# Kernel optimization log

Measured on AMD Instinct MI355X. Metric: run time of the kernel, lower is better.

Reference implementation:

```python
import jax, jax.numpy as jnp
import numpy as np
from jax import lax

H = 192; W = 192; C = 256; N = H * W; E = 294912; K = 289; DSIG = 1
SLOPE = 0.01
EPS = 1e-5


def leaky(x):
    return jnp.where(x >= 0, x, SLOPE * x)


def conv2d(x, w, pad, groups):
    return lax.conv_general_dilated(
        x, w, (1, 1), [(pad, pad), (pad, pad)],
        dimension_numbers=('NCHW', 'OIHW', 'NCHW'),
        feature_group_count=groups)


def bn2d(x, g, b):
    # BatchNorm2d with track_running_stats=False -> always batch stats (biased var)
    m = x.mean(axis=(0, 2, 3), keepdims=True)
    v = x.var(axis=(0, 2, 3), keepdims=True)
    return (x - m) / jnp.sqrt(v + EPS) * g.reshape(1, -1, 1, 1) + b.reshape(1, -1, 1, 1)


def conv_batch(x, w, g, b, pad, groups):
    # nn.Sequential(LeakyReLU(0.01), Conv2d(bias=False), BatchNorm2d)
    return bn2d(conv2d(leaky(x), w, pad, groups), g, b)


def bn1d(x, g, b):
    m = x.mean(axis=0)
    v = x.var(axis=0)
    return (x - m) / jnp.sqrt(v + EPS) * g + b


def setup_inputs() -> dict:
    key = jax.random.key(0)
    ks = jax.random.split(key, 20)
    X = jax.random.normal(ks[0], (N, C), dtype=jnp.float32)
    src = jax.random.randint(ks[1], (E,), 0, N)
    dst = jax.random.randint(ks[2], (E,), 0, N)
    k1 = jax.random.randint(ks[3], (E,), 0, K)
    k2 = jax.random.randint(ks[4], (E,), 0, K)
    InfoIdx = jnp.stack([src, k1, dst, k2], axis=1).astype(jnp.int64)
    edgmsk = (jax.random.uniform(ks[5], (E, 1)) < 0.9).astype(jnp.float32)
    s = 0.05
    inp = {
        'X': X, 'InfoIdx': InfoIdx, 'edgmsk': edgmsk,
        # PPM: depthwise 17x17 conv_batch then 1x1 conv_batch
        'ppm_w0': jax.random.normal(ks[6], (C, 1, 17, 17), jnp.float32) * s,
        'ppm_g0': jnp.ones((C,), jnp.float32), 'ppm_b0': jnp.zeros((C,), jnp.float32),
        'ppm_w1': jax.random.normal(ks[7], (C, C, 1, 1), jnp.float32) * s,
        'ppm_g1': jnp.ones((C,), jnp.float32), 'ppm_b1': jnp.zeros((C,), jnp.float32),
        # FFN_1: two 1x1 conv_batch
        'ffn1_w0': jax.random.normal(ks[8], (C, C, 1, 1), jnp.float32) * s,
        'ffn1_g0': jnp.ones((C,), jnp.float32), 'ffn1_b0': jnp.zeros((C,), jnp.float32),
        'ffn1_w1': jax.random.normal(ks[9], (C, C, 1, 1), jnp.float32) * s,
        'ffn1_g1': jnp.ones((C,), jnp.float32), 'ffn1_b1': jnp.zeros((C,), jnp.float32),
        # Dis: Linear(C,C) -> LeakyReLU -> Linear(C, 289)
        'dis_w1': jax.random.normal(ks[10], (C, C), jnp.float32) * s,
        'dis_b1': jnp.zeros((C,), jnp.float32),
        'dis_w2': jax.random.normal(ks[11], (K * DSIG, C), jnp.float32) * s,
        'dis_b2': jnp.zeros((K * DSIG,), jnp.float32),
        # BatchNorm1d
        'bn_g': jnp.ones((C,), jnp.float32), 'bn_b': jnp.zeros((C,), jnp.float32),
        # FFN_2 = DoubleConv: depthwise-expand 3x3 (groups=C, out=4C) then 1x1
        'ffn2_w0': jax.random.normal(ks[12], (4 * C, 1, 3, 3), jnp.float32) * s,
        'ffn2_g0': jnp.ones((4 * C,), jnp.float32), 'ffn2_b0': jnp.zeros((4 * C,), jnp.float32),
        'ffn2_w1': jax.random.normal(ks[13], (C, 4 * C, 1, 1), jnp.float32) * s,
        'ffn2_g1': jnp.ones((C,), jnp.float32), 'ffn2_b1': jnp.zeros((C,), jnp.float32),
    }
    return inp


def reference(X, InfoIdx, edgmsk,
              ppm_w0, ppm_g0, ppm_b0, ppm_w1, ppm_g1, ppm_b1,
              ffn1_w0, ffn1_g0, ffn1_b0, ffn1_w1, ffn1_g1, ffn1_b1,
              dis_w1, dis_b1, dis_w2, dis_b2, bn_g, bn_b,
              ffn2_w0, ffn2_g0, ffn2_b0, ffn2_w1, ffn2_g1, ffn2_b1):
    src_idx = InfoIdx[:, 0]
    dst_idx = InfoIdx[:, 2]
    # [N,C] -> [1,C,H,W]
    img = X.T.reshape(1, C, H, W)
    # PPM residual
    t = conv_batch(img, ppm_w0, ppm_g0, ppm_b0, pad=8, groups=C)
    t = conv_batch(t, ppm_w1, ppm_g1, ppm_b1, pad=0, groups=1)
    img = img + t
    # FFN_1 residual
    t = conv_batch(img, ffn1_w0, ffn1_g0, ffn1_b0, pad=0, groups=1)
    t = conv_batch(t, ffn1_w1, ffn1_g1, ffn1_b1, pad=0, groups=1)
    img = img + t
    Xn = img.reshape(C, N).T  # [N, C]
    # Dis MLP -> signal [N, 289, d_signal]
    h = leaky(Xn @ dis_w1.T + dis_b1)
    signal = (h @ dis_w2.T + dis_b2).reshape(N, K, DSIG)
    # edge gather + exp/clamp score
    s_src = signal[src_idx, InfoIdx[:, 1]]  # [E, 1]
    s_dst = signal[dst_idx, InfoIdx[:, 3]]  # [E, 1]
    aij = jnp.exp(jnp.clip(s_src + s_dst, -5.0, 5.0)) * edgmsk  # [E, 1]
    # two scatter-sum reductions to dst nodes
    A_sum = jax.ops.segment_sum(aij, dst_idx, num_segments=N)  # [N, 1]
    XA_sum = jax.ops.segment_sum(Xn[src_idx] * aij, dst_idx, num_segments=N)  # [N, C]
    X_trans = XA_sum / (A_sum + 1e-5)
    Xn = Xn + bn1d(X_trans, bn_g, bn_b)
    # FFN_2 = DoubleConv with residual skip
    img = Xn.T.reshape(1, C, H, W)
    t = conv_batch(img, ffn2_w0, ffn2_g0, ffn2_b0, pad=1, groups=C)
    t = conv_batch(t, ffn2_w1, ffn2_g1, ffn2_b1, pad=0, groups=1)
    out = t + img
    return out.reshape(C, N).T  # final bg.ndata['X'], [N, C]
```

## Files before the change

kernel.cpp:

```cpp
#include <hip/hip_runtime.h>
#include <cstddef>

#define HW 192
#define NP 36864
#define CH 256
#define EDGES 294912
#define KSIG 289
#define SLOPE 0.01f
#define BNEPS 1e-5f
#define PADW 208
#define PADSZ (PADW * PADW)

typedef unsigned short u16;
typedef __attribute__((ext_vector_type(8))) short bf16x8;
typedef __attribute__((ext_vector_type(4))) float f32x4;

__device__ __forceinline__ float leaky(float x) { return x >= 0.f ? x : SLOPE * x; }
__device__ __forceinline__ u16 f2bf(float x) {
  unsigned u = __float_as_uint(x);
  unsigned r = (u + 0x7fffu + ((u >> 16) & 1u)) >> 16;
  return (u16)r;
}
__device__ __forceinline__ float bf2f(unsigned h) { return __uint_as_float(h << 16); }
__device__ __forceinline__ void bnss(const float* sums, const float* sqs,
                                     const float* g, const float* b, int k,
                                     float& s, float& h) {
  float mean = sums[k] * (1.f / NP);
  float var = sqs[k] * (1.f / NP) - mean * mean;
  s = g[k] * rsqrtf(var + BNEPS);
  h = b[k] - mean * s;
}

__global__ __launch_bounds__(256) void k_transpose_pad(const float* __restrict__ src,
                                                       float* __restrict__ dst,
                                                       u16* __restrict__ pad) {
  __shared__ float tile[32][33];
  int s0 = blockIdx.x * 32, r0 = blockIdx.y * 32;
  int tx = threadIdx.x & 31, ty = threadIdx.x >> 5;
#pragma unroll
  for (int j = 0; j < 4; j++)
    tile[ty + 8 * j][tx] = src[(size_t)(r0 + ty + 8 * j) * CH + s0 + tx];
  __syncthreads();
  int n = r0 + tx;
  int y = n / HW, x = n - y * HW;
#pragma unroll
  for (int j = 0; j < 4; j++) {
    int c = s0 + ty + 8 * j;
    float v = tile[tx][ty + 8 * j];
    dst[(size_t)c * NP + n] = v;
    pad[(size_t)c * PADSZ + (y + 8) * PADW + x + 8] = f2bf(leaky(v));
  }
}

__global__ __launch_bounds__(256) void k_mkT(const float* __restrict__ w,
                                             u16* __restrict__ Tg) {
  int c = blockIdx.x;
  const float* wc = w + c * 289;
  u16* tc = Tg + (size_t)c * 8704;
  for (int i = threadIdx.x; i < 8704; i += 256) {
    int ky = i >> 9, rem = i & 511, n = rem >> 5, k = rem & 31;
    int kx = k - n;
    float v = (kx >= 0 && kx < 17) ? wc[ky * 17 + kx] : 0.f;
    tc[i] = f2bf(v);
  }
}

__global__ __launch_bounds__(256) void k_cvtW(const float* __restrict__ pw1,
                                              const float* __restrict__ f1w0,
                                              const float* __restrict__ f1w1,
                                              const float* __restrict__ dw1,
                                              const float* __restrict__ dw2,
                                              const float* __restrict__ f2w1,
                                              u16* __restrict__ out) {
  int i = blockIdx.x * 256 + threadIdx.x;
  float v;
  if (i < 65536) v = pw1[i];
  else if (i < 131072) v = f1w0[i - 65536];
  else if (i < 196608) v = f1w1[i - 131072];
  else if (i < 262144) v = dw1[i - 196608];
  else if (i < 360448) { int j = i - 262144; v = (j < KSIG * 256) ? dw2[j] : 0.f; }
  else v = f2w1[i - 360448];
  out[i] = f2bf(v);
}

__global__ __launch_bounds__(256) void k_stats_bf(const u16* __restrict__ Xr,
                                                  float* __restrict__ sums,
                                                  float* __restrict__ sqs) {
  int row = blockIdx.x;
  int t = threadIdx.x;
  const uint4* p = (const uint4*)(Xr + (size_t)row * NP);
  float s = 0.f, q = 0.f;
  for (int i = t; i < NP / 8; i += 256) {
    uint4 v = p[i];
    unsigned w[4] = {v.x, v.y, v.z, v.w};
#pragma unroll
    for (int j = 0; j < 4; j++) {
      float a = bf2f(w[j] & 0xffffu), c = bf2f(w[j] >> 16);
      s += a + c; q += a * a + c * c;
    }
  }
  __shared__ float ss[256], qq[256];
  ss[t] = s; qq[t] = q;
  __syncthreads();
  for (int d = 128; d > 0; d >>= 1) {
    if (t < d) { ss[t] += ss[t + d]; qq[t] += qq[t + d]; }
    __syncthreads();
  }
  if (t == 0) { sums[row] = ss[0]; sqs[row] = qq[0]; }
}

__global__ __launch_bounds__(256) void k_cvtT(const float* __restrict__ in,
                                              u16* __restrict__ outT, int M) {
  __shared__ float tile[32][65];
  int n0 = blockIdx.x * 64, k0 = blockIdx.y * 32;
  int t = threadIdx.x;
#pragma unroll
  for (int i = 0; i < 2; i++) {
    int ci = i * 256 + t;
    int k = ci >> 4, cg = (ci & 15) * 4;
    float4 v = *(const float4*)&in[(size_t)(k0 + k) * NP + n0 + cg];
    tile[k][cg] = v.x; tile[k][cg + 1] = v.y; tile[k][cg + 2] = v.z; tile[k][cg + 3] = v.w;
  }
  __syncthreads();
  int n = t >> 2, kg = (t & 3) * 8;
  uint4 o;
  o.x = (unsigned)f2bf(tile[kg + 0][n]) | ((unsigned)f2bf(tile[kg + 1][n]) << 16);
  o.y = (unsigned)f2bf(tile[kg + 2][n]) | ((unsigned)f2bf(tile[kg + 3][n]) << 16);
  o.z = (unsigned)f2bf(tile[kg + 4][n]) | ((unsigned)f2bf(tile[kg + 5][n]) << 16);
  o.w = (unsigned)f2bf(tile[kg + 6][n]) | ((unsigned)f2bf(tile[kg + 7][n]) << 16);
  *(uint4*)&outT[(size_t)(n0 + n) * M + k0 + kg] = o;
}

__global__ __launch_bounds__(256) void k_cvtT_bf(const u16* __restrict__ in,
                                                 u16* __restrict__ outT,
                                                 const float* __restrict__ sums,
                                                 const float* __restrict__ sqs,
                                                 const float* __restrict__ g,
                                                 const float* __restrict__ b, int M) {
  __shared__ float tile[32][65];
  int n0 = blockIdx.x * 64, k0 = blockIdx.y * 32;
  int t = threadIdx.x;
  int k = t >> 3, cg = (t & 7) * 8;
  float s, h; bnss(sums, sqs, g, b, k0 + k, s, h);
  uint4 v = *(const uint4*)&in[(size_t)(k0 + k) * NP + n0 + cg];
  unsigned w[4] = {v.x, v.y, v.z, v.w};
#pragma unroll
  for (int j = 0; j < 4; j++) {
    tile[k][cg + 2 * j]     = leaky(fmaf(bf2f(w[j] & 0xffffu), s, h));
    tile[k][cg + 2 * j + 1] = leaky(fmaf(bf2f(w[j] >> 16), s, h));
  }
  __syncthreads();
  int n = t >> 2, kg = (t & 3) * 8;
  uint4 o;
  o.x = (unsigned)f2bf(tile[kg + 0][n]) | ((unsigned)f2bf(tile[kg + 1][n]) << 16);
  o.y = (unsigned)f2bf(tile[kg + 2][n]) | ((unsigned)f2bf(tile[kg + 3][n]) << 16);
  o.z = (unsigned)f2bf(tile[kg + 4][n]) | ((unsigned)f2bf(tile[kg + 5][n]) << 16);
  o.w = (unsigned)f2bf(tile[kg + 6][n]) | ((unsigned)f2bf(tile[kg + 7][n]) << 16);
  *(uint4*)&outT[(size_t)(n0 + n) * M + k0 + kg] = o;
}

__global__ __launch_bounds__(256) void k_fuse1(const float* __restrict__ base,
                                               const u16* __restrict__ raw,
                                               const float* __restrict__ sums,
                                               const float* __restrict__ sqs,
                                               const float* __restrict__ g,
                                               const float* __restrict__ b,
                                               float* __restrict__ img2,
                                               u16* __restrict__ outT) {
  __shared__ float tile[32][65];
  int n0 = blockIdx.x * 64, k0 = blockIdx.y * 32;
  int t = threadIdx.x;
#pragma unroll
  for (int i = 0; i < 2; i++) {
    int ci = i * 256 + t;
    int k = ci >> 4, cg = (ci & 15) * 4;
    float s, h; bnss(sums, sqs, g, b, k0 + k, s, h);
    size_t idx = (size_t)(k0 + k) * NP + n0 + cg;
    float4 bv = *(const float4*)&base[idx];
    uint2 rv = *(const uint2*)&raw[idx];
    float r0 = bf2f(rv.x & 0xffffu), r1 = bf2f(rv.x >> 16);
    float r2 = bf2f(rv.y & 0xffffu), r3 = bf2f(rv.y >> 16);
    float4 o;
    o.x = bv.x + fmaf(r0, s, h); o.y = bv.y + fmaf(r1, s, h);
    o.z = bv.z + fmaf(r2, s, h); o.w = bv.w + fmaf(r3, s, h);
    *(float4*)&img2[idx] = o;
    tile[k][cg]     = leaky(o.x);
    tile[k][cg + 1] = leaky(o.y);
    tile[k][cg + 2] = leaky(o.z);
    tile[k][cg + 3] = leaky(o.w);
  }
  __syncthreads();
  int n = t >> 2, kg = (t & 3) * 8;
  uint4 o;
  o.x = (unsigned)f2bf(tile[kg + 0][n]) | ((unsigned)f2bf(tile[kg + 1][n]) << 16);
  o.y = (unsigned)f2bf(tile[kg + 2][n]) | ((unsigned)f2bf(tile[kg + 3][n]) << 16);
  o.z = (unsigned)f2bf(tile[kg + 4][n]) | ((unsigned)f2bf(tile[kg + 5][n]) << 16);
  o.w = (unsigned)f2bf(tile[kg + 6][n]) | ((unsigned)f2bf(tile[kg + 7][n]) << 16);
  *(uint4*)&outT[(size_t)(n0 + n) * CH + k0 + kg] = o;
}

__global__ __launch_bounds__(256) void k_fuse2(const float* __restrict__ base,
                                               const u16* __restrict__ raw,
                                               const float* __restrict__ sums,
                                               const float* __restrict__ sqs,
                                               const float* __restrict__ g,
                                               const float* __restrict__ b,
                                               float* __restrict__ XnT,
                                               u16* __restrict__ outT) {
  __shared__ float tile[32][65];
  int n0 = blockIdx.x * 64, k0 = blockIdx.y * 32;
  int t = threadIdx.x;
#pragma unroll
  for (int i = 0; i < 2; i++) {
    int ci = i * 256 + t;
    int k = ci >> 4, cg = (ci & 15) * 4;
    float s, h; bnss(sums, sqs, g, b, k0 + k, s, h);
    size_t idx = (size_t)(k0 + k) * NP + n0 + cg;
    float4 bv = *(const float4*)&base[idx];
    uint2 rv = *(const uint2*)&raw[idx];
    float r0 = bf2f(rv.x & 0xffffu), r1 = bf2f(rv.x >> 16);
    float r2 = bf2f(rv.y & 0xffffu), r3 = bf2f(rv.y >> 16);
    tile[k][cg]     = bv.x + fmaf(r0, s, h);
    tile[k][cg + 1] = bv.y + fmaf(r1, s, h);
    tile[k][cg + 2] = bv.z + fmaf(r2, s, h);
    tile[k][cg + 3] = bv.w + fmaf(r3, s, h);
  }
  __syncthreads();
  int n = t >> 2, kg = (t & 3) * 8;
  float4 f0 = {tile[kg + 0][n], tile[kg + 1][n], tile[kg + 2][n], tile[kg + 3][n]};
  float4 f1 = {tile[kg + 4][n], tile[kg + 5][n], tile[kg + 6][n], tile[kg + 7][n]};
  *(float4*)&XnT[(size_t)(n0 + n) * CH + k0 + kg] = f0;
  *(float4*)&XnT[(size_t)(n0 + n) * CH + k0 + kg + 4] = f1;
  uint4 o;
  o.x = (unsigned)f2bf(f0.x) | ((unsigned)f2bf(f0.y) << 16);
  o.y = (unsigned)f2bf(f0.z) | ((unsigned)f2bf(f0.w) << 16);
  o.z = (unsigned)f2bf(f1.x) | ((unsigned)f2bf(f1.y) << 16);
  o.w = (unsigned)f2bf(f1.z) | ((unsigned)f2bf(f1.w) << 16);
  *(uint4*)&outT[(size_t)(n0 + n) * CH + k0 + kg] = o;
}

__global__ __launch_bounds__(256) void k_mgemm(const u16* __restrict__ A,
                                               const u16* __restrict__ Bt,
                                               float* __restrict__ Outf,
                                               u16* __restrict__ Outb,
                                               const float* __restrict__ bias,
                                               int K, int Mstore, int actout) {
  __shared__ u16 As[128 * 32];
  __shared__ u16 Bs[128 * 32];
  int t = threadIdx.x;
  int lane = t & 63, wave = t >> 6;
  int wm = (wave >> 1) * 64, wn = (wave & 1) * 64;
  int m0 = blockIdx.y * 128, n0 = blockIdx.x * 128;
  int r = lane & 15, q = lane >> 4;
  f32x4 acc[4][4];
#pragma unroll
  for (int a = 0; a < 4; a++)
#pragma unroll
    for (int b = 0; b < 4; b++) acc[a][b] = (f32x4){0.f, 0.f, 0.f, 0.f};

  for (int k0 = 0; k0 < K; k0 += 32) {
#pragma unroll
    for (int i = 0; i < 2; i++) {
      int cc = t + i * 256;
      int mm = cc >> 2, kq = (cc & 3) * 8;
      uint4 av = *(const uint4*)&A[(size_t)(m0 + mm) * K + k0 + kq];
      uint4 bv = *(const uint4*)&Bt[(size_t)(n0 + mm) * K + k0 + kq];
      *(uint4*)&As[mm * 32 + kq] = av;
      *(uint4*)&Bs[mm * 32 + kq] = bv;
    }
    __syncthreads();
    bf16x8 af[4], bfr[4];
#pragma unroll
    for (int mt = 0; mt < 4; mt++)
      af[mt] = *(const bf16x8*)&As[(wm + mt * 16 + r) * 32 + q * 8];
#pragma unroll
    for (int nt = 0; nt < 4; nt++)
      bfr[nt] = *(const bf16x8*)&Bs[(wn + nt * 16 + r) * 32 + q * 8];
#pragma unroll
    for (int mt = 0; mt < 4; mt++)
#pragma unroll
      for (int nt = 0; nt < 4; nt++)
        acc[mt][nt] = __builtin_amdgcn_mfma_f32_16x16x32_bf16(af[mt], bfr[nt], acc[mt][nt], 0, 0, 0);
    __syncthreads();
  }
#pragma unroll
  for (int mt = 0; mt < 4; mt++) {
    int mrow = m0 + wm + mt * 16 + q * 4;
#pragma unroll
    for (int i = 0; i < 4; i++) {
      int m = mrow + i;
      if (m >= Mstore) continue;
      float bs = bias ? bias[m] : 0.f;
#pragma unroll
      for (int nt = 0; nt < 4; nt++) {
        float v = acc[mt][nt][i] + bs;
        if (actout) v = leaky(v);
        size_t oi = (size_t)m * NP + n0 + wn + nt * 16 + r;
        if (Outb) Outb[oi] = f2bf(v); else Outf[oi] = v;
      }
    }
  }
}

__global__ __launch_bounds__(256) void k_dwconv17(const u16* __restrict__ pad,
                                                  const u16* __restrict__ Tg,
                                                  u16* __restrict__ outb) {
  int c = blockIdx.y;
  int tile = blockIdx.x;
  int ty0 = (tile / 3) * 64, tx0 = (tile % 3) * 64;
  __shared__ u16 smIn[80 * 88];
  __shared__ u16 smT[17 * 16 * 40];
  const u16* pc = pad + (size_t)c * PADSZ;
  for (int cc = threadIdx.x; cc < 800; cc += 256) {
    int rr = cc / 10, j = cc - rr * 10;
    uint4 v = *(const uint4*)(pc + (ty0 + rr) * PADW + tx0 + j * 8);
    *(uint4*)(smIn + rr * 88 + j * 8) = v;
  }
  const u16* tc = Tg + (size_t)c * 8704;
  for (int cc = threadIdx.x; cc < 1088; cc += 256) {
    int rr = cc >> 2, j = cc & 3;
    uint4 v = *(const uint4*)(tc + rr * 32 + j * 8);
    *(uint4*)(smT + rr * 40 + j * 8) = v;
  }
  __syncthreads();
  int lane = threadIdx.x & 63, wave = threadIdx.x >> 6;
  int wy = wave * 16;
  int r = lane & 15, q = lane >> 4;
  f32x4 acc[4];
#pragma unroll
  for (int xt = 0; xt < 4; xt++) acc[xt] = (f32x4){0.f, 0.f, 0.f, 0.f};
#pragma unroll
  for (int ky = 0; ky < 17; ky++) {
    bf16x8 bfrag = *(const bf16x8*)&smT[(ky * 16 + r) * 40 + q * 8];
    int rowA = wy + r + ky;
#pragma unroll
    for (int xt = 0; xt < 4; xt++) {
      bf16x8 afrag = *(const bf16x8*)&smIn[rowA * 88 + xt * 16 + q * 8];
      acc[xt] = __builtin_amdgcn_mfma_f32_16x16x32_bf16(afrag, bfrag, acc[xt], 0, 0, 0);
    }
  }
  u16* oc = outb + (size_t)c * NP;
#pragma unroll
  for (int xt = 0; xt < 4; xt++) {
    int x = tx0 + xt * 16 + r;
#pragma unroll
    for (int i = 0; i < 4; i++) {
      int y = ty0 + wy + q * 4 + i;
      oc[y * HW + x] = f2bf(acc[xt][i]);
    }
  }
}

__global__ __launch_bounds__(256) void k_conv3x4(const float* __restrict__ in,
                                                 const float* __restrict__ w,
                                                 u16* __restrict__ out) {
  int wave = threadIdx.x >> 6, lane = threadIdx.x & 63;
  int c = blockIdx.y;
  int y = blockIdx.x * 4 + wave;
  const float* wc = w + (size_t)(4 * c) * 9;
  float wr[36];
#pragma unroll
  for (int k = 0; k < 36; k++) wr[k] = wc[k];
  float acc[4][3];
#pragma unroll
  for (int oc = 0; oc < 4; oc++)
#pragma unroll
    for (int s = 0; s < 3; s++) acc[oc][s] = 0.f;
  const float* base = in + (size_t)c * NP;
#pragma unroll
  for (int ky = 0; ky < 3; ky++) {
    int ry = y + ky - 1;
    if (ry < 0 || ry >= HW) continue;
    const float* rp = base + ry * HW;
    float a0 = leaky(rp[lane]);
    float a1 = leaky(rp[64 + lane]);
    float a2 = leaky(rp[128 + lane]);
    float e0 = __shfl(a0, 63), e1 = __shfl(a1, 63);
    float b1 = __shfl(a1, 0),  b2 = __shfl(a2, 0);
    float l0 = __shfl_up(a0, 1); if (lane == 0) l0 = 0.f;
    float l1 = __shfl_up(a1, 1); if (lane == 0) l1 = e0;
    float l2 = __shfl_up(a2, 1); if (lane == 0) l2 = e1;
    float r0 = __shfl_down(a0, 1); if (lane == 63) r0 = b1;
    float r1 = __shfl_down(a1, 1); if (lane == 63) r1 = b2;
    float r2 = __shfl_down(a2, 1); if (lane == 63) r2 = 0.f;
#pragma unroll
    for (int oc = 0; oc < 4; oc++) {
      float w0 = wr[oc * 9 + ky * 3], w1 = wr[oc * 9 + ky * 3 + 1], w2 = wr[oc * 9 + ky * 3 + 2];
      acc[oc][0] = fmaf(w0, l0, fmaf(w1, a0, fmaf(w2, r0, acc[oc][0])));
      acc[oc][1] = fmaf(w0, l1, fmaf(w1, a1, fmaf(w2, r1, acc[oc][1])));
      acc[oc][2] = fmaf(w0, l2, fmaf(w1, a2, fmaf(w2, r2, acc[oc][2])));
    }
  }
  size_t ob = (size_t)(4 * c) * NP + (size_t)y * HW + lane;
#pragma unroll
  for (int oc = 0; oc < 4; oc++) {
    out[ob + (size_t)oc * NP]       = f2bf(acc[oc][0]);
    out[ob + (size_t)oc * NP + 64]  = f2bf(acc[oc][1]);
    out[ob + (size_t)oc * NP + 128] = f2bf(acc[oc][2]);
  }
}

__global__ __launch_bounds__(256) void k_edge(const int* __restrict__ info,
                                              const float* __restrict__ msk,
                                              const float* __restrict__ sig,
                                              float* __restrict__ aij,
                                              int* __restrict__ counts) {
  int e = blockIdx.x * 256 + threadIdx.x;
  int4 ii = ((const int4*)info)[e];
  float s = sig[(size_t)ii.y * NP + ii.x] + sig[(size_t)ii.w * NP + ii.z];
  s = fminf(fmaxf(s, -5.f), 5.f);
  aij[e] = expf(s) * msk[e];
  atomicAdd(&counts[ii.z], 1);
}

__global__ __launch_bounds__(256) void k_scan1(const int* __restrict__ counts,
                                               int* __restrict__ offsets,
                                               int* __restrict__ bsum) {
  __shared__ int sm[256];
  int t = threadIdx.x;
  int i = blockIdx.x * 256 + t;
  int v = counts[i];
  sm[t] = v;
  __syncthreads();
  for (int d = 1; d < 256; d <<= 1) {
    int add = (t >= d) ? sm[t - d] : 0;
    __syncthreads();
    sm[t] += add;
    __syncthreads();
  }
  offsets[i] = sm[t] - v;
  if (t == 255) bsum[blockIdx.x] = sm[255];
}
__global__ __launch_bounds__(256) void k_scan2(const int* __restrict__ bsum,
                                               int* __restrict__ boff) {
  __shared__ int sm[256];
  int t = threadIdx.x;
  int v = (t < 144) ? bsum[t] : 0;
  sm[t] = v;
  __syncthreads();
  for (int d = 1; d < 256; d <<= 1) {
    int add = (t >= d) ? sm[t - d] : 0;
    __syncthreads();
    sm[t] += add;
    __syncthreads();
  }
  boff[t] = sm[t] - v;
}
__global__ __launch_bounds__(256) void k_scan3(int* __restrict__ offsets,
                                               const int* __restrict__ boff,
                                               int* __restrict__ cursor) {
  int i = blockIdx.x * 256 + threadIdx.x;
  int o = offsets[i] + boff[blockIdx.x];
  offsets[i] = o;
  cursor[i] = o;
  if (i == 0) offsets[NP] = EDGES;
}
__global__ __launch_bounds__(256) void k_scatter(const int* __restrict__ info,
                                                 int* __restrict__ cursor,
                                                 int* __restrict__ sorted) {
  int e = blockIdx.x * 256 + threadIdx.x;
  int d = info[4 * e + 2];
  int pos = atomicAdd(&cursor[d], 1);
  sorted[pos] = e;
}

__global__ __launch_bounds__(256) void k_agg(const int* __restrict__ offsets,
                                             const int* __restrict__ sorted,
                                             const float* __restrict__ aij,
                                             const int* __restrict__ info,
                                             const u16* __restrict__ XnBf,
                                             float* __restrict__ Xtr) {
  int wave = threadIdx.x >> 6, lane = threadIdx.x & 63;
  int node = blockIdx.x * 4 + wave;
  int o0 = offsets[node], o1 = offsets[node + 1];
  float ax = 0.f, ay = 0.f, az = 0.f, aw = 0.f, asum = 0.f;
  for (int i = o0; i < o1; i++) {
    int e = sorted[i];
    float a = aij[e];
    int s = info[4 * e];
    uint2 v = ((const uint2*)(XnBf + (size_t)s * CH))[lane];
    ax = fmaf(a, bf2f(v.x & 0xffffu), ax);
    ay = fmaf(a, bf2f(v.x >> 16), ay);
    az = fmaf(a, bf2f(v.y & 0xffffu), az);
    aw = fmaf(a, bf2f(v.y >> 16), aw);
    asum += a;
  }
  float inv = 1.f / (asum + 1e-5f);
  float4 o = {ax * inv, ay * inv, az * inv, aw * inv};
  ((float4*)(Xtr + (size_t)node * CH))[lane] = o;
}

__global__ __launch_bounds__(256) void k_colstats(const float* __restrict__ Xt,
                                                  float* __restrict__ sums,
                                                  float* __restrict__ sqs) {
  int c = threadIdx.x;
  float s = 0.f, q = 0.f;
  for (int n = blockIdx.x; n < NP; n += gridDim.x) {
    float v = Xt[(size_t)n * CH + c];
    s += v; q += v * v;
  }
  atomicAdd(&sums[c], s);
  atomicAdd(&sqs[c], q);
}

__global__ __launch_bounds__(256) void k_mkimg4(const float* __restrict__ Xn,
                                                const float* __restrict__ Xtr,
                                                const float* __restrict__ sums,
                                                const float* __restrict__ sqs,
                                                const float* __restrict__ g,
                                                const float* __restrict__ b,
                                                float* __restrict__ img4) {
  __shared__ float tile[32][33];
  int c0 = blockIdx.x * 32, n0 = blockIdx.y * 32;
  int tx = threadIdx.x & 31, ty = threadIdx.x >> 5;
  int c = c0 + tx;
  float s, h; bnss(sums, sqs, g, b, c, s, h);
#pragma unroll
  for (int j = 0; j < 4; j++) {
    size_t idx = (size_t)(n0 + ty + 8 * j) * CH + c;
    tile[ty + 8 * j][tx] = Xn[idx] + fmaf(Xtr[idx], s, h);
  }
  __syncthreads();
#pragma unroll
  for (int j = 0; j < 4; j++) {
    int cc = c0 + ty + 8 * j;
    img4[(size_t)cc * NP + n0 + tx] = tile[tx][ty + 8 * j];
  }
}

__global__ __launch_bounds__(256) void k_final(const u16* __restrict__ raw5,
                                               const float* __restrict__ img4,
                                               const float* __restrict__ sums,
                                               const float* __restrict__ sqs,
                                               const float* __restrict__ g,
                                               const float* __restrict__ b,
                                               float* __restrict__ out) {
  __shared__ float tile[32][33];
  int n0 = blockIdx.x * 32, c0 = blockIdx.y * 32;
  int tx = threadIdx.x & 31, ty = threadIdx.x >> 5;
#pragma unroll
  for (int j = 0; j < 4; j++) {
    int c = c0 + ty + 8 * j;
    float s, h; bnss(sums, sqs, g, b, c, s, h);
    size_t idx = (size_t)c * NP + n0 + tx;
    tile[ty + 8 * j][tx] = fmaf(bf2f(raw5[idx]), s, h) + img4[idx];
  }
  __syncthreads();
#pragma unroll
  for (int j = 0; j < 4; j++) {
    int n = n0 + ty + 8 * j;
    out[(size_t)n * CH + c0 + tx] = tile[tx][ty + 8 * j];
  }
}

extern "C" void kernel_launch(void* const* d_in, const int* in_sizes, int n_in,
                              void* d_out, int out_size, void* d_ws, size_t ws_size,
                              hipStream_t stream) {
  (void)in_sizes; (void)n_in; (void)out_size; (void)ws_size;
  const float* X    = (const float*)d_in[0];
  const int*   info = (const int*)d_in[1];
  const float* msk  = (const float*)d_in[2];
  const float* pw0  = (const float*)d_in[3];
  const float* pg0  = (const float*)d_in[4];
  const float* pb0  = (const float*)d_in[5];
  const float* pw1  = (const float*)d_in[6];
  const float* pg1  = (const float*)d_in[7];
  const float* pb1  = (const float*)d_in[8];
  const float* f1w0 = (const float*)d_in[9];
  const float* f1g0 = (const float*)d_in[10];
  const float* f1b0 = (const float*)d_in[11];
  const float* f1w1 = (const float*)d_in[12];
  const float* f1g1 = (const float*)d_in[13];
  const float* f1b1 = (const float*)d_in[14];
  const float* dw1  = (const float*)d_in[15];
  const float* db1  = (const float*)d_in[16];
  const float* dw2  = (const float*)d_in[17];
  const float* db2  = (const float*)d_in[18];
  const float* bng  = (const float*)d_in[19];
  const float* bnb  = (const float*)d_in[20];
  const float* f2w0 = (const float*)d_in[21];
  const float* f2g0 = (const float*)d_in[22];
  const float* f2b0 = (const float*)d_in[23];
  const float* f2w1 = (const float*)d_in[24];
  const float* f2g1 = (const float*)d_in[25];
  const float* f2b1 = (const float*)d_in[26];
  float* out = (float*)d_out;

  float* ws = (float*)d_ws;
  float* sum0 = ws + 0;    float* sq0 = ws + 256;
  float* sum1 = ws + 512;  float* sq1 = ws + 768;
  float* sum2 = ws + 1024; float* sq2 = ws + 1280;
  float* sum3 = ws + 1536; float* sq3 = ws + 1792;
  float* sum5 = ws + 2048; float* sq5 = ws + 2304;
  float* sumT = ws + 2560; float* sqT = ws + 2816;
  float* sum4 = ws + 3072; float* sq4 = ws + 4096;
  int* counts  = (int*)(ws + 8192);
  int* offsets = (int*)(ws + 45056);
  int* cursor  = (int*)(ws + 82176);
  int* bsum    = (int*)(ws + 119296);
  int* boff    = (int*)(ws + 119552);
  int* sorted  = (int*)(ws + 131072);
  float* aij   = ws + 425984;
  const size_t S = (size_t)NP * CH;
  float* slotD = ws + 720896;
  float* slotB = slotD + S;
  float* slotA = slotB + S;
  float* slotC = slotA + S;
  u16* bfB  = (u16*)(slotC + S);
  u16* bfH  = bfB + S;
  float* sigT = (float*)(bfH + S);
  u16* bfW  = (u16*)(sigT + (size_t)KSIG * NP);
  u16* Ppad = (u16*)slotC;
  u16* Tg   = (u16*)slotD;
  u16* raw4bf  = (u16*)slotB;
  u16* bfT1024 = bfB;
  u16* raw5bf  = (u16*)slotD;

  hipMemsetAsync(ws, 0, 5120 * sizeof(float), stream);
  hipMemsetAsync(counts, 0, NP * sizeof(int), stream);
  hipMemsetAsync(Ppad, 0, (size_t)PADSZ * CH * sizeof(u16), stream);

  dim3 b256(256);
  k_cvtW<<<2432, b256, 0, stream>>>(pw1, f1w0, f1w1, dw1, dw2, f2w1, bfW);
  k_mkT<<<CH, b256, 0, stream>>>(pw0, Tg);
  k_transpose_pad<<<dim3(CH / 32, NP / 32), b256, 0, stream>>>(X, slotA, Ppad);
  k_dwconv17<<<dim3(9, CH), b256, 0, stream>>>(Ppad, Tg, bfH);
  k_stats_bf<<<CH, b256, 0, stream>>>(bfH, sum0, sq0);
  k_cvtT_bf<<<dim3(NP / 64, 8), b256, 0, stream>>>(bfH, bfB, sum0, sq0, pg0, pb0, CH);
  k_mgemm<<<dim3(NP / 128, 2), b256, 0, stream>>>(bfW, bfB, nullptr, bfH, nullptr, CH, CH, 0);
  k_stats_bf<<<CH, b256, 0, stream>>>(bfH, sum1, sq1);
  k_fuse1<<<dim3(NP / 64, 8), b256, 0, stream>>>(slotA, bfH, sum1, sq1, pg1, pb1, slotD, bfB);
  k_mgemm<<<dim3(NP / 128, 2), b256, 0, stream>>>(bfW + 65536, bfB, nullptr, bfH, nullptr, CH, CH, 0);
  k_stats_bf<<<CH, b256, 0, stream>>>(bfH, sum2, sq2);
  k_cvtT_bf<<<dim3(NP / 64, 8), b256, 0, stream>>>(bfH, bfB, sum2, sq2, f1g0, f1b0, CH);
  k_mgemm<<<dim3(NP / 128, 2), b256, 0, stream>>>(bfW + 131072, bfB, nullptr, bfH, nullptr, CH, CH, 0);
  k_stats_bf<<<CH, b256, 0, stream>>>(bfH, sum3, sq3);
  k_fuse2<<<dim3(NP / 64, 8), b256, 0, stream>>>(slotD, bfH, sum3, sq3, f1g1, f1b1, slotA, bfB);
  k_mgemm<<<dim3(NP / 128, 2), b256, 0, stream>>>(bfW + 196608, bfB, slotC, nullptr, db1, CH, CH, 1);
  k_cvtT<<<dim3(NP / 64, 8), b256, 0, stream>>>(slotC, bfH, CH);
  k_mgemm<<<dim3(NP / 128, 3), b256, 0, stream>>>(bfW + 262144, bfH, sigT, nullptr, db2, CH, KSIG, 0);
  k_edge<<<EDGES / 256, b256, 0, stream>>>(info, msk, sigT, aij, counts);
  k_scan1<<<NP / 256, b256, 0, stream>>>(counts, offsets, bsum);
  k_scan2<<<1, b256, 0, stream>>>(bsum, boff);
  k_scan3<<<NP / 256, b256, 0, stream>>>(offsets, boff, cursor);
  k_scatter<<<EDGES / 256, b256, 0, stream>>>(info, cursor, sorted);
  k_agg<<<NP / 4, b256, 0, stream>>>(offsets, sorted, aij, info, bfB, slotD);
  k_colstats<<<288, b256, 0, stream>>>(slotD, sumT, sqT);
  k_mkimg4<<<dim3(CH / 32, NP / 32), b256, 0, stream>>>(slotA, slotD, sumT, sqT, bng, bnb, slotC);
  k_conv3x4<<<dim3(48, CH), b256, 0, stream>>>(slotC, f2w0, raw4bf);
  k_stats_bf<<<1024, b256, 0, stream>>>(raw4bf, sum4, sq4);
  k_cvtT_bf<<<dim3(NP / 64, 32), b256, 0, stream>>>(raw4bf, bfT1024, sum4, sq4, f2g0, f2b0, 1024);
  k_mgemm<<<dim3(NP / 128, 2), b256, 0, stream>>>(bfW + 360448, bfT1024, nullptr, raw5bf, nullptr, 1024, CH, 0);
  k_stats_bf<<<CH, b256, 0, stream>>>(raw5bf, sum5, sq5);
  k_final<<<dim3(NP / 32, CH / 32), b256, 0, stream>>>(raw5bf, slotC, sum5, sq5, f2g1, f2b1, out);
}
```

Baseline: 676.6 us.

## Presort edge src/weights in scatter, widen aggregation loads, store X_trans as bf16

```diff
diff --git a/kernel.cpp b/kernel.cpp
--- a/kernel.cpp
+++ b/kernel.cpp
@@ -456,47 +456,78 @@
   if (i == 0) offsets[NP] = EDGES;
 }
 __global__ __launch_bounds__(256) void k_scatter(const int* __restrict__ info,
+                                                 const float* __restrict__ aij,
                                                  int* __restrict__ cursor,
-                                                 int* __restrict__ sorted) {
+                                                 int* __restrict__ srcs,
+                                                 float* __restrict__ aijw) {
   int e = blockIdx.x * 256 + threadIdx.x;
-  int d = info[4 * e + 2];
-  int pos = atomicAdd(&cursor[d], 1);
-  sorted[pos] = e;
+  int4 ii = ((const int4*)info)[e];
+  int pos = atomicAdd(&cursor[ii.z], 1);
+  srcs[pos] = ii.x;
+  aijw[pos] = aij[e];
 }
 
 __global__ __launch_bounds__(256) void k_agg(const int* __restrict__ offsets,
-                                             const int* __restrict__ sorted,
-                                             const float* __restrict__ aij,
-                                             const int* __restrict__ info,
+                                             const int* __restrict__ srcs,
+                                             const float* __restrict__ aijw,
                                              const u16* __restrict__ XnBf,
-                                             float* __restrict__ Xtr) {
+                                             u16* __restrict__ XtrBf) {
   int wave = threadIdx.x >> 6, lane = threadIdx.x & 63;
   int node = blockIdx.x * 4 + wave;
   int o0 = offsets[node], o1 = offsets[node + 1];
-  float ax = 0.f, ay = 0.f, az = 0.f, aw = 0.f, asum = 0.f;
-  for (int i = o0; i < o1; i++) {
-    int e = sorted[i];
-    float a = aij[e];
-    int s = info[4 * e];
-    uint2 v = ((const uint2*)(XnBf + (size_t)s * CH))[lane];
-    ax = fmaf(a, bf2f(v.x & 0xffffu), ax);
-    ay = fmaf(a, bf2f(v.x >> 16), ay);
-    az = fmaf(a, bf2f(v.y & 0xffffu), az);
-    aw = fmaf(a, bf2f(v.y >> 16), aw);
+  int half = lane >> 5, l32 = lane & 31;
+  float acc[8] = {0.f, 0.f, 0.f, 0.f, 0.f, 0.f, 0.f, 0.f};
+  float asum = 0.f;
+  int i = o0 + half;
+  for (; i + 2 < o1; i += 4) {
+    int s0 = srcs[i], s1 = srcs[i + 2];
+    float a0 = aijw[i], a1 = aijw[i + 2];
+    uint4 v0 = ((const uint4*)(XnBf + (size_t)s0 * CH))[l32];
+    uint4 v1 = ((const uint4*)(XnBf + (size_t)s1 * CH))[l32];
+    unsigned w0[4] = {v0.x, v0.y, v0.z, v0.w};
+    unsigned w1[4] = {v1.x, v1.y, v1.z, v1.w};
+#pragma unroll
+    for (int j = 0; j < 4; j++) {
+      acc[2 * j]     = fmaf(a0, bf2f(w0[j] & 0xffffu), acc[2 * j]);
+      acc[2 * j + 1] = fmaf(a0, bf2f(w0[j] >> 16),     acc[2 * j + 1]);
+      acc[2 * j]     = fmaf(a1, bf2f(w1[j] & 0xffffu), acc[2 * j]);
+      acc[2 * j + 1] = fmaf(a1, bf2f(w1[j] >> 16),     acc[2 * j + 1]);
+    }
+    asum += a0 + a1;
+  }
+  for (; i < o1; i += 2) {
+    int s = srcs[i];
+    float a = aijw[i];
+    uint4 v = ((const uint4*)(XnBf + (size_t)s * CH))[l32];
+    unsigned w[4] = {v.x, v.y, v.z, v.w};
+#pragma unroll
+    for (int j = 0; j < 4; j++) {
+      acc[2 * j]     = fmaf(a, bf2f(w[j] & 0xffffu), acc[2 * j]);
+      acc[2 * j + 1] = fmaf(a, bf2f(w[j] >> 16),     acc[2 * j + 1]);
+    }
     asum += a;
   }
-  float inv = 1.f / (asum + 1e-5f);
-  float4 o = {ax * inv, ay * inv, az * inv, aw * inv};
-  ((float4*)(Xtr + (size_t)node * CH))[lane] = o;
-}
-
-__global__ __launch_bounds__(256) void k_colstats(const float* __restrict__ Xt,
+#pragma unroll
+  for (int j = 0; j < 8; j++) acc[j] += __shfl_xor(acc[j], 32, 64);
+  asum += __shfl_xor(asum, 32, 64);
+  if (half == 0) {
+    float inv = 1.f / (asum + 1e-5f);
+    uint4 o;
+    o.x = (unsigned)f2bf(acc[0] * inv) | ((unsigned)f2bf(acc[1] * inv) << 16);
+    o.y = (unsigned)f2bf(acc[2] * inv) | ((unsigned)f2bf(acc[3] * inv) << 16);
+    o.z = (unsigned)f2bf(acc[4] * inv) | ((unsigned)f2bf(acc[5] * inv) << 16);
+    o.w = (unsigned)f2bf(acc[6] * inv) | ((unsigned)f2bf(acc[7] * inv) << 16);
+    ((uint4*)(XtrBf + (size_t)node * CH))[l32] = o;
+  }
+}
+
+__global__ __launch_bounds__(256) void k_colstats(const u16* __restrict__ Xt,
                                                   float* __restrict__ sums,
                                                   float* __restrict__ sqs) {
   int c = threadIdx.x;
   float s = 0.f, q = 0.f;
   for (int n = blockIdx.x; n < NP; n += gridDim.x) {
-    float v = Xt[(size_t)n * CH + c];
+    float v = bf2f(Xt[(size_t)n * CH + c]);
     s += v; q += v * v;
   }
   atomicAdd(&sums[c], s);
@@ -504,7 +535,7 @@
 }
 
 __global__ __launch_bounds__(256) void k_mkimg4(const float* __restrict__ Xn,
-                                                const float* __restrict__ Xtr,
+                                                const u16* __restrict__ XtrBf,
                                                 const float* __restrict__ sums,
                                                 const float* __restrict__ sqs,
                                                 const float* __restrict__ g,
@@ -518,7 +549,7 @@
 #pragma unroll
   for (int j = 0; j < 4; j++) {
     size_t idx = (size_t)(n0 + ty + 8 * j) * CH + c;
-    tile[ty + 8 * j][tx] = Xn[idx] + fmaf(Xtr[idx], s, h);
+    tile[ty + 8 * j][tx] = Xn[idx] + fmaf(bf2f(XtrBf[idx]), s, h);
   }
   __syncthreads();
 #pragma unroll
@@ -599,7 +630,7 @@
   int* cursor  = (int*)(ws + 82176);
   int* bsum    = (int*)(ws + 119296);
   int* boff    = (int*)(ws + 119552);
-  int* sorted  = (int*)(ws + 131072);
+  int* srcs    = (int*)(ws + 131072);
   float* aij   = ws + 425984;
   const size_t S = (size_t)NP * CH;
   float* slotD = ws + 720896;
@@ -610,11 +641,13 @@
   u16* bfH  = bfB + S;
   float* sigT = (float*)(bfH + S);
   u16* bfW  = (u16*)(sigT + (size_t)KSIG * NP);
+  float* aijw = (float*)(bfW + 622592);
   u16* Ppad = (u16*)slotC;
   u16* Tg   = (u16*)slotD;
   u16* raw4bf  = (u16*)slotB;
   u16* bfT1024 = bfB;
-  u16* raw5bf  = (u16*)slotD;
+  u16* XtrBf   = (u16*)slotD;
+  u16* raw5bf  = (u16*)slotB;
 
   hipMemsetAsync(ws, 0, 5120 * sizeof(float), stream);
   hipMemsetAsync(counts, 0, NP * sizeof(int), stream);
@@ -643,10 +676,10 @@
   k_scan1<<<NP / 256, b256, 0, stream>>>(counts, offsets, bsum);
   k_scan2<<<1, b256, 0, stream>>>(bsum, boff);
   k_scan3<<<NP / 256, b256, 0, stream>>>(offsets, boff, cursor);
-  k_scatter<<<EDGES / 256, b256, 0, stream>>>(info, cursor, sorted);
-  k_agg<<<NP / 4, b256, 0, stream>>>(offsets, sorted, aij, info, bfB, slotD);
-  k_colstats<<<288, b256, 0, stream>>>(slotD, sumT, sqT);
-  k_mkimg4<<<dim3(CH / 32, NP / 32), b256, 0, stream>>>(slotA, slotD, sumT, sqT, bng, bnb, slotC);
+  k_scatter<<<EDGES / 256, b256, 0, stream>>>(info, aij, cursor, srcs, aijw);
+  k_agg<<<NP / 4, b256, 0, stream>>>(offsets, srcs, aijw, bfB, XtrBf);
+  k_colstats<<<288, b256, 0, stream>>>(XtrBf, sumT, sqT);
+  k_mkimg4<<<dim3(CH / 32, NP / 32), b256, 0, stream>>>(slotA, XtrBf, sumT, sqT, bng, bnb, slotC);
   k_conv3x4<<<dim3(48, CH), b256, 0, stream>>>(slotC, f2w0, raw4bf);
   k_stats_bf<<<1024, b256, 0, stream>>>(raw4bf, sum4, sq4);
   k_cvtT_bf<<<dim3(NP / 64, 32), b256, 0, stream>>>(raw4bf, bfT1024, sum4, sq4, f2g0, f2b0, 1024);
```

Result: faster. 648.3 us (-4.2%).
